# Kernel tuning notes

Measured on AMD Instinct MI355X. Metric: run time of the kernel, lower is better.

Reference implementation:

```python
import jax, jax.numpy as jnp
import numpy as np

N_VARS = 16
BATCH = 16
SEQ = 512
P = N_VARS * (N_VARS - 1)  # ordered pairs i != j


def setup_inputs() -> dict:
    key = jax.random.key(0)
    ks = jax.random.split(key, 12)
    n = N_VARS

    def w(k, shape, fan_in):
        return jax.random.normal(k, shape, dtype=jnp.float32) / np.sqrt(fan_in)

    z = lambda *s: jnp.zeros(s, jnp.float32)
    return {
        'data': jax.random.normal(ks[0], (BATCH, SEQ, n), dtype=jnp.float32),
        # structure learner: n*n -> 256 -> 128 -> n*n (dropout skipped / eval mode)
        'Ws1': w(ks[1], (n * n, 256), n * n), 'bs1': z(256),
        'Ws2': w(ks[2], (256, 128), 256), 'bs2': z(128),
        'Ws3': w(ks[3], (128, n * n), 128), 'bs3': z(n * n),
        # per-variable causal mechanisms (stacked): (n-1) -> 128 -> 64 -> 1
        'Wm1': w(ks[4], (n, n - 1, 128), n - 1), 'bm1': z(n, 128),
        'Wm2': w(ks[5], (n, 128, 64), 128), 'bm2': z(n, 64),
        'Wm3': w(ks[6], (n, 64), 64), 'bm3': z(n),
        # per-pair independence tests (stacked): 2 -> 32 -> 1, sigmoid
        'Wt1': w(ks[7], (P, 2, 32), 2), 'bt1': z(P, 32),
        'Wt2': w(ks[8], (P, 32), 32), 'bt2': z(P),
    }


def reference(data, Ws1, bs1, Ws2, bs2, Ws3, bs3,
              Wm1, bm1, Wm2, bm2, Wm3, bm3,
              Wt1, bt1, Wt2, bt2):
    B, S, n = data.shape
    N = B * S
    flat = data.reshape(N, n)  # [N, n] all samples

    # ---- correlations of batch-averaged series (vectorized corrcoef) ----
    avg = data.mean(axis=0)                    # [S, n]
    xc = avg - avg.mean(axis=0, keepdims=True)
    cov = xc.T @ xc                            # [n, n]
    std = jnp.sqrt(jnp.clip(jnp.diag(cov), 0.0))
    denom = std[:, None] * std[None, :]
    corr = jnp.abs(jnp.where(denom > 0, cov / jnp.where(denom > 0, denom, 1.0), 0.0))
    corr = corr * (1.0 - jnp.eye(n, dtype=corr.dtype))  # zero diagonal (i != j only)

    # ---- structure learner MLP -> sigmoid -> strict upper-tri DAG mask ----
    h = jax.nn.relu(corr.reshape(1, -1) @ Ws1 + bs1)
    h = jax.nn.relu(h @ Ws2 + bs2)
    adj = jax.nn.sigmoid(h @ Ws3 + bs3).reshape(n, n)
    adj = jnp.triu(adj, 1)

    # ---- causal mechanisms: gather-parents -> per-var MLP -> scatter ----
    idx = np.stack([[j for j in range(n) if j != v] for v in range(n)])  # [n, n-1]
    pmask = adj > 0.5
    parent_mask = pmask[idx, np.arange(n)[:, None]].astype(flat.dtype)   # [n, n-1]
    inp = flat[:, idx] * parent_mask[None]                               # [N, n, n-1]
    h1 = jax.nn.relu(jnp.einsum('nvp,vph->nvh', inp, Wm1) + bm1)         # [N, n, 128]
    h2 = jax.nn.relu(jnp.einsum('nvh,vhk->nvk', h1, Wm2) + bm2)          # [N, n, 64]
    mech = jnp.einsum('nvk,vk->nv', h2, Wm3) + bm3                       # [N, n]
    has_parents = parent_mask.sum(axis=1) > 0                            # [n]
    predictions = jnp.where(has_parents[None, :], mech, flat).reshape(B, S, n)

    # ---- batched per-pair independence tests ----
    pairs = np.array([(i, j) for i in range(n) for j in range(n) if i != j])
    pi, pj = pairs[:, 0], pairs[:, 1]
    X = jnp.stack([flat[:, pi], flat[:, pj]], axis=-1)                   # [N, P, 2]
    ht = jax.nn.relu(jnp.einsum('npc,pch->nph', X, Wt1) + bt1)           # [N, P, 32]
    s = jax.nn.sigmoid(jnp.einsum('nph,ph->np', ht, Wt2) + bt2).mean(axis=0)  # [P]
    scores = jnp.zeros((n, n), flat.dtype).at[pi, pj].set(s)

    return adj, predictions, scores
```

## Files before the change

kernel.cpp:

```cpp
#include <hip/hip_runtime.h>
#include <hip/hip_bf16.h>


typedef __attribute__((ext_vector_type(8))) short bf16x8;
typedef __attribute__((ext_vector_type(4))) short bf16x4;
typedef __attribute__((ext_vector_type(4))) float f32x4;

#define DEV __device__ __forceinline__
DEV short f2bf(float f){ __hip_bfloat16 h = __float2bfloat16(f); short s; __builtin_memcpy(&s,&h,2); return s; }

struct GraphSm {
    float avT[16 * 532];
    float part[512];
    float corr[256];
    float h1[256];
    float h2[128];
    float adj[256];
};
struct MechSm {
    short W2T[64 * 136];
    short H1[8][16 * 136];
    float W1[16 * 128];
    float B1[128];
    float B2[64];
    float W3[64];
};
struct PairSm {
    float w0[32], w1[32], bb[32], w2[32];
    float red[512];
    float b2s;
};
union SmU { GraphSm g; MechSm m; PairSm p; };

__global__ void __launch_bounds__(512, 2) k_fused(
    const float* __restrict__ data,
    const float* __restrict__ Ws1, const float* __restrict__ bs1,
    const float* __restrict__ Ws2, const float* __restrict__ bs2,
    const float* __restrict__ Ws3, const float* __restrict__ bs3,
    const float* __restrict__ Wm1, const float* __restrict__ bm1,
    const float* __restrict__ Wm2, const float* __restrict__ bm2,
    const float* __restrict__ Wm3, const float* __restrict__ bm3,
    const float* __restrict__ Wt1, const float* __restrict__ bt1,
    const float* __restrict__ Wt2, const float* __restrict__ bt2,
    float* __restrict__ out)
{
    __shared__ __align__(16) SmU sm;
    int tid = threadIdx.x, bid = blockIdx.x;

    if (bid >= 128) {
        int p = bid - 128;
        int i = p / 15, jr = p % 15;
        int j = jr + (jr >= i ? 1 : 0);
        if (tid < 32) {
            sm.p.w0[tid] = Wt1[p*64 + tid];
            sm.p.w1[tid] = Wt1[p*64 + 32 + tid];
            sm.p.bb[tid] = bt1[p*32 + tid];
            sm.p.w2[tid] = Wt2[p*32 + tid];
        }
        if (tid == 0) sm.p.b2s = bt2[p];
        __syncthreads();
        float b2sv = sm.p.b2s;
        float acc = 0.f;
        float nxa = data[tid*16 + i];
        float nxb = data[tid*16 + j];
        for (int it = 0; it < 16; ++it) {
            float xa = nxa, xb = nxb;
            if (it < 15) {
                int sn = (it+1)*512 + tid;
                nxa = data[sn*16 + i];
                nxb = data[sn*16 + j];
            }
            float za = 0.f, zb = 0.f;
            #pragma unroll
            for (int h = 0; h < 32; h += 2) {
                float t1 = fmaf(xa, sm.p.w0[h],   fmaf(xb, sm.p.w1[h],   sm.p.bb[h]));
                za = fmaf(fmaxf(t1, 0.f), sm.p.w2[h],   za);
                float t2 = fmaf(xa, sm.p.w0[h+1], fmaf(xb, sm.p.w1[h+1], sm.p.bb[h+1]));
                zb = fmaf(fmaxf(t2, 0.f), sm.p.w2[h+1], zb);
            }
            float z = b2sv + za + zb;
            acc += __builtin_amdgcn_rcpf(1.f + __expf(-z));
        }
        sm.p.red[tid] = acc;
        __syncthreads();
        for (int off = 256; off > 0; off >>= 1) {
            if (tid < off) sm.p.red[tid] += sm.p.red[tid + off];
            __syncthreads();
        }
        if (tid == 0) out[256 + 131072 + i*16 + j] = sm.p.red[0] * (1.f/8192.f);
        return;
    }

    int v = bid >> 3, chunk = bid & 7;
    int gs0 = chunk * 1024;

    float pf_wm1[4];
    {
        #pragma unroll
        for (int r = 0; r < 4; ++r) {
            int e = tid + 512*r;
            int k = e >> 7, h = e & 127;
            pf_wm1[r] = 0.f;
            if (k != v) {
                int p = k - (k > v ? 1 : 0);
                pf_wm1[r] = Wm1[v*1920 + p*128 + h];
            }
        }
    }
    float4 pf_wm2[4];
    {
        const float* wp = Wm2 + v*8192 + tid*16;
        #pragma unroll
        for (int m4 = 0; m4 < 4; ++m4) pf_wm2[m4] = *(const float4*)&wp[m4*4];
    }
    float b1r  = bm1[v*128 + (tid & 127)];
    float b2r_ = bm2[v*64  + (tid & 63)];
    float w3r  = Wm3[v*64  + (tid & 63)];
    float bm3v = bm3[v];
    float bs1r = bs1[tid & 255];
    float bs2r = bs2[tid & 127];
    float bs3r = bs3[tid & 255];

    {
        int vb = (tid & 3) * 4, sg = tid >> 2;
        for (int k = 0; k < 4; ++k) {
            int s = sg + k*128;
            float ax=0.f, ay=0.f, az=0.f, aw=0.f;
            #pragma unroll
            for (int b = 0; b < 16; ++b) {
                float4 d4 = *(const float4*)&data[b*8192 + s*16 + vb];
                ax += d4.x; ay += d4.y; az += d4.z; aw += d4.w;
            }
            sm.g.avT[(vb+0)*532 + s] = ax * 0.0625f;
            sm.g.avT[(vb+1)*532 + s] = ay * 0.0625f;
            sm.g.avT[(vb+2)*532 + s] = az * 0.0625f;
            sm.g.avT[(vb+3)*532 + s] = aw * 0.0625f;
        }
    }
    __syncthreads();
    if (tid < 128) {
        int vv = tid >> 3, sgm = tid & 7;
        const float* rp = &sm.g.avT[vv*532 + sgm*64];
        float a0=0.f, a1=0.f, a2=0.f, a3=0.f;
        for (int s = 0; s < 64; s += 4) {
            float4 fa = *(const float4*)&rp[s];
            a0 += fa.x; a1 += fa.y; a2 += fa.z; a3 += fa.w;
        }
        sm.g.h2[tid] = (a0+a1)+(a2+a3);
    }
    __syncthreads();
    int ci, cj; float mci, mcj;
    {
        int t = tid & 255, hh = tid >> 8;
        ci = t >> 4; cj = t & 15;
        mci = 0.f; mcj = 0.f;
        #pragma unroll
        for (int q = 0; q < 8; ++q) { mci += sm.g.h2[ci*8 + q]; mcj += sm.g.h2[cj*8 + q]; }
        mci *= (1.f/512.f); mcj *= (1.f/512.f);
        const float* pi_ = &sm.g.avT[ci*532 + hh*256];
        const float* pj_ = &sm.g.avT[cj*532 + hh*256];
        float a0=0.f, a1=0.f, a2=0.f, a3=0.f;
        #pragma unroll 8
        for (int s = 0; s < 256; s += 4) {
            float4 fa = *(const float4*)&pi_[s];
            float4 fb = *(const float4*)&pj_[s];
            a0 = fmaf(fa.x, fb.x, a0); a1 = fmaf(fa.y, fb.y, a1);
            a2 = fmaf(fa.z, fb.z, a2); a3 = fmaf(fa.w, fb.w, a3);
        }
        sm.g.part[tid] = (a0+a1)+(a2+a3);
    }
    __syncthreads();
    if (tid < 256) {
        float cij = sm.g.part[tid] + sm.g.part[256 + tid] - 512.f*mci*mcj;
        float cii = sm.g.part[ci*17] + sm.g.part[256 + ci*17] - 512.f*mci*mci;
        float cjj = sm.g.part[cj*17] + sm.g.part[256 + cj*17] - 512.f*mcj*mcj;
        float den = sqrtf(fmaxf(cii, 0.f)) * sqrtf(fmaxf(cjj, 0.f));
        sm.g.corr[tid] = (den > 0.f && ci != cj) ? fabsf(cij/den) : 0.f;
    }
    __syncthreads();

    float* red2 = sm.g.avT;

    {
        int o4 = tid & 63, ks = tid >> 6;
        const float* W1p = Ws1 + ks*32*256 + o4*4;
        const float* cp  = sm.g.corr + ks*32;
        float ax=0.f, ay=0.f, az=0.f, aw=0.f;
        float bx=0.f, by=0.f, bz=0.f, bw=0.f;
        #pragma unroll 8
        for (int i = 0; i < 32; i += 2) {
            float4 w0 = *(const float4*)&W1p[(i  )*256];
            float4 w1 = *(const float4*)&W1p[(i+1)*256];
            float c0 = cp[i], c1 = cp[i+1];
            ax=fmaf(c0,w0.x,ax); ay=fmaf(c0,w0.y,ay); az=fmaf(c0,w0.z,az); aw=fmaf(c0,w0.w,aw);
            bx=fmaf(c1,w1.x,bx); by=fmaf(c1,w1.y,by); bz=fmaf(c1,w1.z,bz); bw=fmaf(c1,w1.w,bw);
        }
        float4 r4; r4.x=ax+bx; r4.y=ay+by; r4.z=az+bz; r4.w=aw+bw;
        *(float4*)&red2[ks*256 + o4*4] = r4;
    }
    __syncthreads();
    if (tid < 256) {
        float s = bs1r;
        #pragma unroll
        for (int k2 = 0; k2 < 8; ++k2) s += red2[k2*256 + tid];
        sm.g.h1[tid] = fmaxf(s, 0.f);
    }
    __syncthreads();
    {
        int o4 = tid & 31, ks = tid >> 5;
        const float* W2p = Ws2 + ks*16*128 + o4*4;
        const float* cp  = sm.g.h1 + ks*16;
        float ax=0.f, ay=0.f, az=0.f, aw=0.f;
        float bx=0.f, by=0.f, bz=0.f, bw=0.f;
        #pragma unroll
        for (int i = 0; i < 16; i += 2) {
            float4 w0 = *(const float4*)&W2p[(i  )*128];
            float4 w1 = *(const float4*)&W2p[(i+1)*128];
            float c0 = cp[i], c1 = cp[i+1];
            ax=fmaf(c0,w0.x,ax); ay=fmaf(c0,w0.y,ay); az=fmaf(c0,w0.z,az); aw=fmaf(c0,w0.w,aw);
            bx=fmaf(c1,w1.x,bx); by=fmaf(c1,w1.y,by); bz=fmaf(c1,w1.z,bz); bw=fmaf(c1,w1.w,bw);
        }
        float4 r4; r4.x=ax+bx; r4.y=ay+by; r4.z=az+bz; r4.w=aw+bw;
        *(float4*)&red2[ks*128 + o4*4] = r4;
    }
    __syncthreads();
    if (tid < 128) {
        float s = bs2r;
        #pragma unroll
        for (int k2 = 0; k2 < 16; ++k2) s += red2[k2*128 + tid];
        sm.g.h2[tid] = fmaxf(s, 0.f);
    }
    __syncthreads();
    {
        int o4 = tid & 63, ks = tid >> 6;
        const float* W3p = Ws3 + ks*16*256 + o4*4;
        const float* cp  = sm.g.h2 + ks*16;
        float ax=0.f, ay=0.f, az=0.f, aw=0.f;
        float bx=0.f, by=0.f, bz=0.f, bw=0.f;
        #pragma unroll
        for (int i = 0; i < 16; i += 2) {
            float4 w0 = *(const float4*)&W3p[(i  )*256];
            float4 w1 = *(const float4*)&W3p[(i+1)*256];
            float c0 = cp[i], c1 = cp[i+1];
            ax=fmaf(c0,w0.x,ax); ay=fmaf(c0,w0.y,ay); az=fmaf(c0,w0.z,az); aw=fmaf(c0,w0.w,aw);
            bx=fmaf(c1,w1.x,bx); by=fmaf(c1,w1.y,by); bz=fmaf(c1,w1.z,bz); bw=fmaf(c1,w1.w,bw);
        }
        float4 r4; r4.x=ax+bx; r4.y=ay+by; r4.z=az+bz; r4.w=aw+bw;
        *(float4*)&red2[ks*256 + o4*4] = r4;
    }
    __syncthreads();
    if (tid < 256) {
        float z = bs3r;
        #pragma unroll
        for (int k2 = 0; k2 < 8; ++k2) z += red2[k2*256 + tid];
        float a = 1.f / (1.f + expf(-z));
        int r = tid >> 4, cc = tid & 15;
        float adjv = (r < cc) ? a : 0.f;
        sm.g.adj[tid] = adjv;
        if (bid == 0) out[tid] = adjv;
    }
    if (bid == 0 && tid >= 256 && tid < 272)
        out[256 + 131072 + (tid-256)*17] = 0.f;
    __syncthreads();

    #pragma unroll
    for (int r = 0; r < 4; ++r) {
        int e = tid + 512*r;
        int k = e >> 7;
        float val = 0.f;
        if (k != v && sm.g.adj[k*16 + v] > 0.5f) val = pf_wm1[r];
        sm.m.W1[e] = val;
    }
    float hp = 0.f;
    #pragma unroll
    for (int k = 0; k < 16; ++k)
        if (k != v && sm.g.adj[k*16 + v] > 0.5f) hp = 1.f;
    #pragma unroll
    for (int m4 = 0; m4 < 4; ++m4) {
        float4 w4 = pf_wm2[m4];
        int e0 = tid*16 + m4*4;
        int h = e0 >> 6;
        int jj0 = e0 & 63;
        sm.m.W2T[(jj0+0)*136 + h] = f2bf(w4.x);
        sm.m.W2T[(jj0+1)*136 + h] = f2bf(w4.y);
        sm.m.W2T[(jj0+2)*136 + h] = f2bf(w4.z);
        sm.m.W2T[(jj0+3)*136 + h] = f2bf(w4.w);
    }
    if (tid < 128) sm.m.B1[tid] = b1r;
    else if (tid < 192) sm.m.B2[tid - 128] = b2r_;
    else if (tid < 256) sm.m.W3[tid - 192] = w3r;
    __syncthreads();

    int lane = tid & 63, wid = tid >> 6;
    int c = lane & 15, q = lane >> 4;

    bf16x8 a1f[8];
    #pragma unroll
    for (int ht = 0; ht < 8; ++ht) {
        #pragma unroll
        for (int jj = 0; jj < 8; ++jj) {
            int k = q*8 + jj;
            float w = (k < 16) ? sm.m.W1[k*128 + ht*16 + c] : 0.f;
            a1f[ht][jj] = f2bf(w);
        }
    }
    bf16x8 b2r[16];
    #pragma unroll
    for (int jt = 0; jt < 4; ++jt)
        #pragma unroll
        for (int ks = 0; ks < 4; ++ks)
            b2r[jt*4 + ks] = *(const bf16x8*)&sm.m.W2T[(jt*16 + c)*136 + ks*32 + q*8];
    float w3c[4], b2c[4];
    #pragma unroll
    for (int jt = 0; jt < 4; ++jt) { w3c[jt] = sm.m.W3[jt*16 + c]; b2c[jt] = sm.m.B2[jt*16 + c]; }

    short* h1buf = sm.m.H1[wid];
    bool act = (q < 2);

    float4 u0c, u1c;
    {
        int st0 = wid*8;
        if (act) {
            const float* xp = &data[(gs0 + st0*16 + c)*16 + q*8];
            u0c = *(const float4*)xp;
            u1c = *(const float4*)(xp + 4);
        }
    }

    for (int stl = 0; stl < 8; ++stl) {
        int st = wid*8 + stl;
        float4 u0 = u0c, u1 = u1c;
        if (stl < 7 && act) {
            const float* xp = &data[(gs0 + (st+1)*16 + c)*16 + q*8];
            u0c = *(const float4*)xp;
            u1c = *(const float4*)(xp + 4);
        }
        bf16x8 xb;
        #pragma unroll
        for (int i2 = 0; i2 < 8; ++i2) xb[i2] = 0;
        if (act) {
            xb[0] = f2bf(u0.x); xb[1] = f2bf(u0.y);
            xb[2] = f2bf(u0.z); xb[3] = f2bf(u0.w);
            xb[4] = f2bf(u1.x); xb[5] = f2bf(u1.y);
            xb[6] = f2bf(u1.z); xb[7] = f2bf(u1.w);
        }
        f32x4 c1[8];
        #pragma unroll
        for (int ht = 0; ht < 8; ++ht) c1[ht] = *(const f32x4*)&sm.m.B1[ht*16 + q*4];
        #pragma unroll
        for (int ht = 0; ht < 8; ++ht)
            c1[ht] = __builtin_amdgcn_mfma_f32_16x16x32_bf16(a1f[ht], xb, c1[ht], 0, 0, 0);
        #pragma unroll
        for (int ht = 0; ht < 8; ++ht) {
            bf16x4 pk;
            #pragma unroll
            for (int r = 0; r < 4; ++r) pk[r] = f2bf(fmaxf(c1[ht][r], 0.f));
            *(bf16x4*)&h1buf[c*136 + ht*16 + q*4] = pk;
        }
        f32x4 c2[4];
        #pragma unroll
        for (int jt = 0; jt < 4; ++jt) {
            float bi = b2c[jt];
            c2[jt] = (f32x4){bi, bi, bi, bi};
        }
        #pragma unroll
        for (int ks = 0; ks < 4; ++ks) {
            bf16x8 a2 = *(const bf16x8*)&h1buf[c*136 + ks*32 + q*8];
            #pragma unroll
            for (int jt = 0; jt < 4; ++jt)
                c2[jt] = __builtin_amdgcn_mfma_f32_16x16x32_bf16(a2, b2r[jt*4 + ks], c2[jt], 0, 0, 0);
        }
        float part[4];
        #pragma unroll
        for (int r = 0; r < 4; ++r) part[r] = 0.f;
        #pragma unroll
        for (int jt = 0; jt < 4; ++jt)
            #pragma unroll
            for (int r = 0; r < 4; ++r)
                part[r] = fmaf(fmaxf(c2[jt][r], 0.f), w3c[jt], part[r]);
        #pragma unroll
        for (int off = 1; off < 16; off <<= 1)
            #pragma unroll
            for (int r = 0; r < 4; ++r)
                part[r] += __shfl_xor(part[r], off, 16);
        if (c == 0) {
            #pragma unroll
            for (int r = 0; r < 4; ++r) {
                int s_loc = st*16 + q*4 + r;
                float mech = part[r] + bm3v;
                float xv = data[(gs0 + s_loc)*16 + v];
                out[256 + (gs0 + s_loc)*16 + v] = (hp != 0.f) ? mech : xv;
            }
        }
    }
}

extern "C" void kernel_launch(void* const* d_in, const int* in_sizes, int n_in,
                              void* d_out, int out_size, void* d_ws, size_t ws_size,
                              hipStream_t stream)
{
    const float* data = (const float*)d_in[0];
    const float* Ws1  = (const float*)d_in[1];
    const float* bs1  = (const float*)d_in[2];
    const float* Ws2  = (const float*)d_in[3];
    const float* bs2  = (const float*)d_in[4];
    const float* Ws3  = (const float*)d_in[5];
    const float* bs3  = (const float*)d_in[6];
    const float* Wm1  = (const float*)d_in[7];
    const float* bm1  = (const float*)d_in[8];
    const float* Wm2  = (const float*)d_in[9];
    const float* bm2  = (const float*)d_in[10];
    const float* Wm3  = (const float*)d_in[11];
    const float* bm3  = (const float*)d_in[12];
    const float* Wt1  = (const float*)d_in[13];
    const float* bt1  = (const float*)d_in[14];
    const float* Wt2  = (const float*)d_in[15];
    const float* bt2  = (const float*)d_in[16];
    float* out = (float*)d_out;
    (void)d_ws; (void)ws_size; (void)in_sizes; (void)n_in; (void)out_size;

    hipLaunchKernelGGL(k_fused, dim3(368), dim3(512), 0, stream,
                       data, Ws1, bs1, Ws2, bs2, Ws3, bs3,
                       Wm1, bm1, Wm2, bm2, Wm3, bm3,
                       Wt1, bt1, Wt2, bt2, out);
}
```

Baseline: 115.5 us.

## Process two pairs per pair-test block and stagger per-block access offsets

Each independence-test block now evaluates two pairs at once, cutting the grid from 368 to 248 blocks and sharing the data loads and the reduction barriers between both pairs. Each block also starts its sample loop at a block-dependent rotation, and the graph/MLP stages rotate their starting row and column offsets by block index. The rotations spread simultaneous accesses to the same addresses across blocks, since all 128 mechanism blocks redundantly read the same weights and data. In exchange, each pair block does twice the serial work and uses more registers.

```diff
diff --git a/kernel.cpp b/kernel.cpp
--- a/kernel.cpp
+++ b/kernel.cpp
@@ -26,9 +26,9 @@
     float W3[64];
 };
 struct PairSm {
-    float w0[32], w1[32], bb[32], w2[32];
-    float red[512];
-    float b2s;
+    float w0[2][32], w1[2][32], bb[2][32], w2[2][32];
+    float red[2][512];
+    float b2s[2];
 };
 union SmU { GraphSm g; MechSm m; PairSm p; };
 
@@ -48,46 +48,68 @@
     int tid = threadIdx.x, bid = blockIdx.x;
 
     if (bid >= 128) {
-        int p = bid - 128;
-        int i = p / 15, jr = p % 15;
-        int j = jr + (jr >= i ? 1 : 0);
-        if (tid < 32) {
-            sm.p.w0[tid] = Wt1[p*64 + tid];
-            sm.p.w1[tid] = Wt1[p*64 + 32 + tid];
-            sm.p.bb[tid] = bt1[p*32 + tid];
-            sm.p.w2[tid] = Wt2[p*32 + tid];
-        }
-        if (tid == 0) sm.p.b2s = bt2[p];
+        int pb = bid - 128;
+        int p0 = pb*2, p1 = p0 + 1;
+        int i0 = p0 / 15, jr0 = p0 % 15;
+        int j0 = jr0 + (jr0 >= i0 ? 1 : 0);
+        int i1 = p1 / 15, jr1 = p1 % 15;
+        int j1 = jr1 + (jr1 >= i1 ? 1 : 0);
+        if (tid < 64) {
+            int pp = tid >> 5, h = tid & 31;
+            int p = pb*2 + pp;
+            sm.p.w0[pp][h] = Wt1[p*64 + h];
+            sm.p.w1[pp][h] = Wt1[p*64 + 32 + h];
+            sm.p.bb[pp][h] = bt1[p*32 + h];
+            sm.p.w2[pp][h] = Wt2[p*32 + h];
+        }
+        if (tid < 2) sm.p.b2s[tid] = bt2[pb*2 + tid];
         __syncthreads();
-        float b2sv = sm.p.b2s;
-        float acc = 0.f;
-        float nxa = data[tid*16 + i];
-        float nxb = data[tid*16 + j];
+        float b2s0 = sm.p.b2s[0], b2s1 = sm.p.b2s[1];
+        float acc0 = 0.f, acc1 = 0.f;
+        float nxa0, nxb0, nxa1, nxb1;
+        {
+            int s = ((bid & 15) * 512) + tid;
+            nxa0 = data[s*16 + i0]; nxb0 = data[s*16 + j0];
+            nxa1 = data[s*16 + i1]; nxb1 = data[s*16 + j1];
+        }
         for (int it = 0; it < 16; ++it) {
-            float xa = nxa, xb = nxb;
+            float xa0 = nxa0, xb0 = nxb0, xa1 = nxa1, xb1 = nxb1;
             if (it < 15) {
-                int sn = (it+1)*512 + tid;
-                nxa = data[sn*16 + i];
-                nxb = data[sn*16 + j];
-            }
-            float za = 0.f, zb = 0.f;
+                int s = (((it + 1 + bid) & 15) * 512) + tid;
+                nxa0 = data[s*16 + i0]; nxb0 = data[s*16 + j0];
+                nxa1 = data[s*16 + i1]; nxb1 = data[s*16 + j1];
+            }
+            float za0=0.f, zb0=0.f, za1=0.f, zb1=0.f;
             #pragma unroll
             for (int h = 0; h < 32; h += 2) {
-                float t1 = fmaf(xa, sm.p.w0[h],   fmaf(xb, sm.p.w1[h],   sm.p.bb[h]));
-                za = fmaf(fmaxf(t1, 0.f), sm.p.w2[h],   za);
-                float t2 = fmaf(xa, sm.p.w0[h+1], fmaf(xb, sm.p.w1[h+1], sm.p.bb[h+1]));
-                zb = fmaf(fmaxf(t2, 0.f), sm.p.w2[h+1], zb);
-            }
-            float z = b2sv + za + zb;
-            acc += __builtin_amdgcn_rcpf(1.f + __expf(-z));
-        }
-        sm.p.red[tid] = acc;
+                float t00 = fmaf(xa0, sm.p.w0[0][h],   fmaf(xb0, sm.p.w1[0][h],   sm.p.bb[0][h]));
+                za0 = fmaf(fmaxf(t00, 0.f), sm.p.w2[0][h],   za0);
+                float t01 = fmaf(xa0, sm.p.w0[0][h+1], fmaf(xb0, sm.p.w1[0][h+1], sm.p.bb[0][h+1]));
+                zb0 = fmaf(fmaxf(t01, 0.f), sm.p.w2[0][h+1], zb0);
+                float t10 = fmaf(xa1, sm.p.w0[1][h],   fmaf(xb1, sm.p.w1[1][h],   sm.p.bb[1][h]));
+                za1 = fmaf(fmaxf(t10, 0.f), sm.p.w2[1][h],   za1);
+                float t11 = fmaf(xa1, sm.p.w0[1][h+1], fmaf(xb1, sm.p.w1[1][h+1], sm.p.bb[1][h+1]));
+                zb1 = fmaf(fmaxf(t11, 0.f), sm.p.w2[1][h+1], zb1);
+            }
+            float z0 = b2s0 + za0 + zb0;
+            float z1 = b2s1 + za1 + zb1;
+            acc0 += __builtin_amdgcn_rcpf(1.f + __expf(-z0));
+            acc1 += __builtin_amdgcn_rcpf(1.f + __expf(-z1));
+        }
+        sm.p.red[0][tid] = acc0;
+        sm.p.red[1][tid] = acc1;
         __syncthreads();
         for (int off = 256; off > 0; off >>= 1) {
-            if (tid < off) sm.p.red[tid] += sm.p.red[tid + off];
+            if (tid < off) {
+                sm.p.red[0][tid] += sm.p.red[0][tid + off];
+                sm.p.red[1][tid] += sm.p.red[1][tid + off];
+            }
             __syncthreads();
         }
-        if (tid == 0) out[256 + 131072 + i*16 + j] = sm.p.red[0] * (1.f/8192.f);
+        if (tid == 0) {
+            out[256 + 131072 + i0*16 + j0] = sm.p.red[0][0] * (1.f/8192.f);
+            out[256 + 131072 + i1*16 + j1] = sm.p.red[1][0] * (1.f/8192.f);
+        }
         return;
     }
 
@@ -122,9 +144,10 @@
     float bs3r = bs3[tid & 255];
 
     {
-        int vb = (tid & 3) * 4, sg = tid >> 2;
+        int vb = (tid & 3) * 4;
+        int sgr = ((tid >> 2) + bid*4) & 127;
         for (int k = 0; k < 4; ++k) {
-            int s = sg + k*128;
+            int s = sgr + k*128;
             float ax=0.f, ay=0.f, az=0.f, aw=0.f;
             #pragma unroll
             for (int b = 0; b < 16; ++b) {
@@ -183,7 +206,8 @@
 
     {
         int o4 = tid & 63, ks = tid >> 6;
-        const float* W1p = Ws1 + ks*32*256 + o4*4;
+        int o4e = (o4 + bid*4) & 63;
+        const float* W1p = Ws1 + ks*32*256 + o4e*4;
         const float* cp  = sm.g.corr + ks*32;
         float ax=0.f, ay=0.f, az=0.f, aw=0.f;
         float bx=0.f, by=0.f, bz=0.f, bw=0.f;
@@ -196,7 +220,7 @@
             bx=fmaf(c1,w1.x,bx); by=fmaf(c1,w1.y,by); bz=fmaf(c1,w1.z,bz); bw=fmaf(c1,w1.w,bw);
         }
         float4 r4; r4.x=ax+bx; r4.y=ay+by; r4.z=az+bz; r4.w=aw+bw;
-        *(float4*)&red2[ks*256 + o4*4] = r4;
+        *(float4*)&red2[ks*256 + o4e*4] = r4;
     }
     __syncthreads();
     if (tid < 256) {
@@ -208,7 +232,8 @@
     __syncthreads();
     {
         int o4 = tid & 31, ks = tid >> 5;
-        const float* W2p = Ws2 + ks*16*128 + o4*4;
+        int o4e = (o4 + bid*2) & 31;
+        const float* W2p = Ws2 + ks*16*128 + o4e*4;
         const float* cp  = sm.g.h1 + ks*16;
         float ax=0.f, ay=0.f, az=0.f, aw=0.f;
         float bx=0.f, by=0.f, bz=0.f, bw=0.f;
@@ -221,7 +246,7 @@
             bx=fmaf(c1,w1.x,bx); by=fmaf(c1,w1.y,by); bz=fmaf(c1,w1.z,bz); bw=fmaf(c1,w1.w,bw);
         }
         float4 r4; r4.x=ax+bx; r4.y=ay+by; r4.z=az+bz; r4.w=aw+bw;
-        *(float4*)&red2[ks*128 + o4*4] = r4;
+        *(float4*)&red2[ks*128 + o4e*4] = r4;
     }
     __syncthreads();
     if (tid < 128) {
@@ -233,7 +258,8 @@
     __syncthreads();
     {
         int o4 = tid & 63, ks = tid >> 6;
-        const float* W3p = Ws3 + ks*16*256 + o4*4;
+        int o4e = (o4 + bid*4) & 63;
+        const float* W3p = Ws3 + ks*16*256 + o4e*4;
         const float* cp  = sm.g.h2 + ks*16;
         float ax=0.f, ay=0.f, az=0.f, aw=0.f;
         float bx=0.f, by=0.f, bz=0.f, bw=0.f;
@@ -246,7 +272,7 @@
             bx=fmaf(c1,w1.x,bx); by=fmaf(c1,w1.y,by); bz=fmaf(c1,w1.z,bz); bw=fmaf(c1,w1.w,bw);
         }
         float4 r4; r4.x=ax+bx; r4.y=ay+by; r4.z=az+bz; r4.w=aw+bw;
-        *(float4*)&red2[ks*256 + o4*4] = r4;
+        *(float4*)&red2[ks*256 + o4e*4] = r4;
     }
     __syncthreads();
     if (tid < 256) {
@@ -419,7 +445,7 @@
     float* out = (float*)d_out;
     (void)d_ws; (void)ws_size; (void)in_sizes; (void)n_in; (void)out_size;
 
-    hipLaunchKernelGGL(k_fused, dim3(368), dim3(512), 0, stream,
+    hipLaunchKernelGGL(k_fused, dim3(248), dim3(512), 0, stream,
                        data, Ws1, bs1, Ws2, bs2, Ws3, bs3,
                        Wm1, bm1, Wm2, bm2, Wm3, bm3,
                        Wt1, bt1, Wt2, bt2, out);
```

Measured after the change: 126.3 us. +9.3%, slower.
